# Kernel tuning notes

Hardware: AMD Instinct MI355X
Metric: run time of the kernel (lower is better)

The kernel has to match this reference:

```python
import jax, jax.numpy as jnp
import numpy as np

LMAX = 3
N_NODES = 100000
C_IN = 128
C_OUT = 128
M = (LMAX + 1) ** 2  # 16 spherical components
# l index for each m component: m in [l^2, (l+1)^2) belongs to l
L_OF_M = np.array([int(np.floor(np.sqrt(m))) for m in range(M)], dtype=np.int32)


def setup_inputs() -> dict:
    key = jax.random.key(0)
    kx, kw = jax.random.split(key)
    x = jax.random.normal(kx, (N_NODES, M, C_IN), dtype=jnp.float32)
    weights = jax.random.normal(kw, (LMAX + 1, C_IN, C_OUT), dtype=jnp.float32)
    return {"x": x, "weights": weights}


def reference(x, weights):
    # x: [N, M, C_in]; weights: [L+1, C_in, C_out]
    # e3nn path_weight for a single-path linear: 1/sqrt(fan_in)
    pw = 1.0 / jnp.sqrt(jnp.asarray(C_IN, dtype=x.dtype))
    w_m = weights[jnp.asarray(L_OF_M)]  # [M, C_in, C_out] gathered per m-component
    # block-diagonal (per-l) matmul, same weight shared across the 2l+1 m's of each l
    y = jnp.einsum('nmc,mcd->nmd', x, w_m) * pw
    return y
```

## Files before the change

### kernel.cpp

```cpp
#include <hip/hip_runtime.h>


typedef __bf16 bf16x8 __attribute__((ext_vector_type(8)));
typedef float f32x4 __attribute__((ext_vector_type(4)));
typedef unsigned short u16x8 __attribute__((ext_vector_type(8)));

#define N_NODES 100000
#define MCOMP 16
#define CIN 128
#define ROWSTRIDE (MCOMP * CIN)

__device__ __forceinline__ unsigned short f2b(float f) {
    unsigned int u = __float_as_uint(f);
    unsigned int r = (u + 0x7fffu + ((u >> 16) & 1u)) >> 16;
    return (unsigned short)r;
}

__global__ void prep_weights(const float* __restrict__ w,
                             unsigned short* __restrict__ wt) {
    int idx = blockIdx.x * blockDim.x + threadIdx.x;
    int l = idx >> 14;
    int rem = idx & 16383;
    int d = rem >> 7;
    int c = rem & 127;
    const float pw = 0.08838834764831845f;
    wt[idx] = f2b(w[(l << 14) + (c << 7) + d] * pw);
}

__global__ __launch_bounds__(256, 4) void linear_mfma(
        const float* __restrict__ x,
        const unsigned short* __restrict__ wt,
        float* __restrict__ y) {
    __shared__ float lds0[32 * 128];
    __shared__ float lds1[32 * 128];

    const int m = blockIdx.y;
    const int l = (m >= 9) ? 3 : (m >= 4) ? 2 : (m >= 1) ? 1 : 0;
    const int wid = threadIdx.x >> 6;
    const int lane = threadIdx.x & 63;
    const int lr = lane & 15;
    const int lk = lane >> 4;
    const int nbase = blockIdx.x * 128;

    const unsigned short* wl = wt + (l << 14);
    bf16x8 wf[2][4];
#pragma unroll
    for (int df = 0; df < 2; ++df)
#pragma unroll
        for (int kk = 0; kk < 4; ++kk)
            wf[df][kk] = __builtin_bit_cast(bf16x8, *(const u16x8*)(
                wl + (((wid * 32 + df * 16 + lr) << 7) + kk * 32 + lk * 8)));

    auto stage = [&](float* buf, int h) {
        const int hbase = nbase + h * 32;
#pragma unroll
        for (int j = 0; j < 4; ++j) {
            int seg = wid * 4 + j;
            int row = seg * 2 + (lane >> 5);
            int slot = (lane & 31) ^ (row & 7);
            const float* src = x + (size_t)(hbase + row) * ROWSTRIDE
                               + m * CIN + slot * 4;
            __builtin_amdgcn_global_load_lds(
                (const __attribute__((address_space(1))) void*)src,
                (__attribute__((address_space(3))) void*)(buf + seg * 256),
                16, 0, 0);
        }
    };

    auto comp = [&](const float* buf, int h) {
        f32x4 acc[2][2];
#pragma unroll
        for (int rf = 0; rf < 2; ++rf)
#pragma unroll
            for (int df = 0; df < 2; ++df)
                acc[rf][df] = (f32x4){0.f, 0.f, 0.f, 0.f};

#pragma unroll
        for (int kk = 0; kk < 4; ++kk) {
#pragma unroll
            for (int rf = 0; rf < 2; ++rf) {
                int row = rf * 16 + lr;
                int sw = row & 7;
                const float* rbase = buf + row * 128 + kk * 32;
                f32x4 v0 = *(const f32x4*)(rbase + ((lk * 2) ^ sw) * 4);
                f32x4 v1 = *(const f32x4*)(rbase + ((lk * 2 + 1) ^ sw) * 4);
                bf16x8 xb;
#pragma unroll
                for (int jj = 0; jj < 4; ++jj) {
                    xb[jj] = (__bf16)v0[jj];
                    xb[jj + 4] = (__bf16)v1[jj];
                }
                acc[rf][0] = __builtin_amdgcn_mfma_f32_16x16x32_bf16(
                    wf[0][kk], xb, acc[rf][0], 0, 0, 0);
                acc[rf][1] = __builtin_amdgcn_mfma_f32_16x16x32_bf16(
                    wf[1][kk], xb, acc[rf][1], 0, 0, 0);
            }
        }
        const int hbase = nbase + h * 32;
#pragma unroll
        for (int rf = 0; rf < 2; ++rf)
#pragma unroll
            for (int df = 0; df < 2; ++df) {
                float* yp = y + (size_t)(hbase + rf * 16 + lr) * ROWSTRIDE
                            + m * CIN + wid * 32 + df * 16 + lk * 4;
                *(f32x4*)yp = acc[rf][df];
            }
    };

    if (nbase + 128 <= N_NODES) {
        stage(lds0, 0);
        asm volatile("s_waitcnt vmcnt(0)" ::: "memory");
        __builtin_amdgcn_s_barrier();

        stage(lds1, 1);
        __builtin_amdgcn_sched_barrier(0);
        comp(lds0, 0);
        asm volatile("s_waitcnt vmcnt(4)" ::: "memory");
        __builtin_amdgcn_s_barrier();

        stage(lds0, 2);
        __builtin_amdgcn_sched_barrier(0);
        comp(lds1, 1);
        asm volatile("s_waitcnt vmcnt(4)" ::: "memory");
        __builtin_amdgcn_s_barrier();

        stage(lds1, 3);
        __builtin_amdgcn_sched_barrier(0);
        comp(lds0, 2);
        asm volatile("s_waitcnt vmcnt(4)" ::: "memory");
        __builtin_amdgcn_s_barrier();

        comp(lds1, 3);
    } else {
        stage(lds0, 0);
        asm volatile("s_waitcnt vmcnt(0)" ::: "memory");
        __builtin_amdgcn_s_barrier();
        comp(lds0, 0);
    }
}

extern "C" void kernel_launch(void* const* d_in, const int* in_sizes, int n_in,
                              void* d_out, int out_size, void* d_ws, size_t ws_size,
                              hipStream_t stream) {
    const float* x = (const float*)d_in[0];
    const float* w = (const float*)d_in[1];
    float* y = (float*)d_out;
    unsigned short* wt = (unsigned short*)d_ws;

    prep_weights<<<256, 256, 0, stream>>>(w, wt);

    dim3 grid((N_NODES + 127) / 128, MCOMP);
    linear_mfma<<<grid, 256, 0, stream>>>(x, wt, y);
}
```

Measured before the change: 341.9 us.

## Replace fixed two-buffer schedule with a looped four-buffer prefetch pipeline

The GEMM kernel now processes 16-row tiles, 16 per block, in a loop. It keeps a ring of four LDS buffers and prefetches three tiles ahead, with the vmcnt wait level chosen per iteration. This replaces the hand-unrolled two-buffer, four-stage schedule over 32-row tiles and halves the number of blocks. The aim is to keep more global loads in flight per wave so load latency is hidden in this bandwidth-bound kernel. The cost is fewer blocks, more complex wait-count bookkeeping that now has to account for stores, and smaller MFMA work per tile.

```diff
diff --git a/kernel.cpp b/kernel.cpp
--- a/kernel.cpp
+++ b/kernel.cpp
@@ -9,6 +9,9 @@
 #define MCOMP 16
 #define CIN 128
 #define ROWSTRIDE (MCOMP * CIN)
+#define TROWS 16
+#define TPB 16
+#define DEPTH 3
 
 __device__ __forceinline__ unsigned short f2b(float f) {
     unsigned int u = __float_as_uint(f);
@@ -31,8 +34,7 @@
         const float* __restrict__ x,
         const unsigned short* __restrict__ wt,
         float* __restrict__ y) {
-    __shared__ float lds0[32 * 128];
-    __shared__ float lds1[32 * 128];
+    __shared__ float lds[4][TROWS * CIN];
 
     const int m = blockIdx.y;
     const int l = (m >= 9) ? 3 : (m >= 4) ? 2 : (m >= 1) ? 1 : 0;
@@ -40,7 +42,8 @@
     const int lane = threadIdx.x & 63;
     const int lr = lane & 15;
     const int lk = lane >> 4;
-    const int nbase = blockIdx.x * 128;
+    const int nbase0 = blockIdx.x * (TROWS * TPB);
+    const int NT = min(TPB, (N_NODES - nbase0) / TROWS);
 
     const unsigned short* wl = wt + (l << 14);
     bf16x8 wf[2][4];
@@ -51,11 +54,12 @@
             wf[df][kk] = __builtin_bit_cast(bf16x8, *(const u16x8*)(
                 wl + (((wid * 32 + df * 16 + lr) << 7) + kk * 32 + lk * 8)));
 
-    auto stage = [&](float* buf, int h) {
-        const int hbase = nbase + h * 32;
+    auto stage = [&](int t) {
+        float* buf = lds[t & 3];
+        const int hbase = nbase0 + t * TROWS;
 #pragma unroll
-        for (int j = 0; j < 4; ++j) {
-            int seg = wid * 4 + j;
+        for (int j = 0; j < 2; ++j) {
+            int seg = wid * 2 + j;
             int row = seg * 2 + (lane >> 5);
             int slot = (lane & 31) ^ (row & 7);
             const float* src = x + (size_t)(hbase + row) * ROWSTRIDE
@@ -67,75 +71,51 @@
         }
     };
 
-    auto comp = [&](const float* buf, int h) {
-        f32x4 acc[2][2];
-#pragma unroll
-        for (int rf = 0; rf < 2; ++rf)
-#pragma unroll
-            for (int df = 0; df < 2; ++df)
-                acc[rf][df] = (f32x4){0.f, 0.f, 0.f, 0.f};
-
+    auto comp = [&](int t) {
+        const float* buf = lds[t & 3];
+        f32x4 acc0 = (f32x4){0.f, 0.f, 0.f, 0.f};
+        f32x4 acc1 = (f32x4){0.f, 0.f, 0.f, 0.f};
+        const int sw = lr & 7;
+        const float* rbase = buf + lr * CIN;
 #pragma unroll
         for (int kk = 0; kk < 4; ++kk) {
+            f32x4 v0 = *(const f32x4*)(rbase + kk * 32 + ((lk * 2) ^ sw) * 4);
+            f32x4 v1 = *(const f32x4*)(rbase + kk * 32 + ((lk * 2 + 1) ^ sw) * 4);
+            bf16x8 xb;
 #pragma unroll
-            for (int rf = 0; rf < 2; ++rf) {
-                int row = rf * 16 + lr;
-                int sw = row & 7;
-                const float* rbase = buf + row * 128 + kk * 32;
-                f32x4 v0 = *(const f32x4*)(rbase + ((lk * 2) ^ sw) * 4);
-                f32x4 v1 = *(const f32x4*)(rbase + ((lk * 2 + 1) ^ sw) * 4);
-                bf16x8 xb;
-#pragma unroll
-                for (int jj = 0; jj < 4; ++jj) {
-                    xb[jj] = (__bf16)v0[jj];
-                    xb[jj + 4] = (__bf16)v1[jj];
-                }
-                acc[rf][0] = __builtin_amdgcn_mfma_f32_16x16x32_bf16(
-                    wf[0][kk], xb, acc[rf][0], 0, 0, 0);
-                acc[rf][1] = __builtin_amdgcn_mfma_f32_16x16x32_bf16(
-                    wf[1][kk], xb, acc[rf][1], 0, 0, 0);
+            for (int jj = 0; jj < 4; ++jj) {
+                xb[jj] = (__bf16)v0[jj];
+                xb[jj + 4] = (__bf16)v1[jj];
             }
+            acc0 = __builtin_amdgcn_mfma_f32_16x16x32_bf16(wf[0][kk], xb, acc0, 0, 0, 0);
+            acc1 = __builtin_amdgcn_mfma_f32_16x16x32_bf16(wf[1][kk], xb, acc1, 0, 0, 0);
         }
-        const int hbase = nbase + h * 32;
-#pragma unroll
-        for (int rf = 0; rf < 2; ++rf)
-#pragma unroll
-            for (int df = 0; df < 2; ++df) {
-                float* yp = y + (size_t)(hbase + rf * 16 + lr) * ROWSTRIDE
-                            + m * CIN + wid * 32 + df * 16 + lk * 4;
-                *(f32x4*)yp = acc[rf][df];
-            }
+        const int hbase = nbase0 + t * TROWS;
+        float* yp = y + (size_t)(hbase + lr) * ROWSTRIDE + m * CIN
+                    + wid * 32 + lk * 4;
+        *(f32x4*)yp = acc0;
+        *(f32x4*)(yp + 16) = acc1;
     };
 
-    if (nbase + 128 <= N_NODES) {
-        stage(lds0, 0);
-        asm volatile("s_waitcnt vmcnt(0)" ::: "memory");
+    stage(0);
+    stage(1);
+    stage(2);
+
+    for (int t = 0; t < NT; ++t) {
+        int vm = 4 + 2 * t;
+        int ve = 6 + 2 * (NT - 1 - t);
+        if (ve < vm) vm = ve;
+        if (vm > 10) vm = 10;
+        switch (vm) {
+            case 4:  asm volatile("s_waitcnt vmcnt(4)" ::: "memory"); break;
+            case 6:  asm volatile("s_waitcnt vmcnt(6)" ::: "memory"); break;
+            case 8:  asm volatile("s_waitcnt vmcnt(8)" ::: "memory"); break;
+            default: asm volatile("s_waitcnt vmcnt(10)" ::: "memory"); break;
+        }
         __builtin_amdgcn_s_barrier();
-
-        stage(lds1, 1);
         __builtin_amdgcn_sched_barrier(0);
-        comp(lds0, 0);
-        asm volatile("s_waitcnt vmcnt(4)" ::: "memory");
-        __builtin_amdgcn_s_barrier();
-
-        stage(lds0, 2);
-        __builtin_amdgcn_sched_barrier(0);
-        comp(lds1, 1);
-        asm volatile("s_waitcnt vmcnt(4)" ::: "memory");
-        __builtin_amdgcn_s_barrier();
-
-        stage(lds1, 3);
-        __builtin_amdgcn_sched_barrier(0);
-        comp(lds0, 2);
-        asm volatile("s_waitcnt vmcnt(4)" ::: "memory");
-        __builtin_amdgcn_s_barrier();
-
-        comp(lds1, 3);
-    } else {
-        stage(lds0, 0);
-        asm volatile("s_waitcnt vmcnt(0)" ::: "memory");
-        __builtin_amdgcn_s_barrier();
-        comp(lds0, 0);
+        if (t + DEPTH < NT) stage(t + DEPTH);
+        comp(t);
     }
 }
 
@@ -149,6 +129,6 @@
 
     prep_weights<<<256, 256, 0, stream>>>(w, wt);
 
-    dim3 grid((N_NODES + 127) / 128, MCOMP);
+    dim3 grid((N_NODES + TROWS * TPB - 1) / (TROWS * TPB), MCOMP);
     linear_mfma<<<grid, 256, 0, stream>>>(x, wt, y);
 }
```

Result: slower. 387.2 us (+13.3%).
